# Kernel tuning notes

Measured on AMD Instinct MI355X. Metric: run time of the kernel, lower is better.

The kernel has to match this reference:

```python
import jax, jax.numpy as jnp
import numpy as np
import math

D_MODEL, N_HEADS, D_K, D_V = 512, 2, 64, 64
C_CLIP = 10.0
MASK_FILL = -10.0

def setup_inputs() -> dict:
    key = jax.random.key(0)
    ks = jax.random.split(key, 12)
    B, Lq, Lk = 4, 2048, 2048
    s = 1.0 / math.sqrt(D_MODEL)
    return {
        "Q": jax.random.normal(ks[0], (B, Lq, D_MODEL), jnp.float32),
        "K": jax.random.normal(ks[1], (B, Lk, D_MODEL), jnp.float32),
        "V": jax.random.normal(ks[2], (B, Lk, D_MODEL), jnp.float32),
        "mask": jax.random.randint(ks[3], (B, Lk), 0, 2) > 0,
        "Wq": jax.random.normal(ks[4], (D_MODEL, N_HEADS * D_K), jnp.float32) * s,
        "bq": jnp.zeros((N_HEADS * D_K,), jnp.float32),
        "Wk": jax.random.normal(ks[5], (D_MODEL, N_HEADS * D_K), jnp.float32) * s,
        "bk": jnp.zeros((N_HEADS * D_K,), jnp.float32),
        "Wv": jax.random.normal(ks[6], (D_MODEL, N_HEADS * D_V), jnp.float32) * s,
        "bv": jnp.zeros((N_HEADS * D_V,), jnp.float32),
        "Wo": jax.random.normal(ks[7], (N_HEADS * D_V, D_MODEL), jnp.float32) * s,
        "bo": jnp.zeros((D_MODEL,), jnp.float32),
    }

def reference(Q, K, V, mask, Wq, bq, Wk, bk, Wv, bv, Wo, bo):
    B, Lq, _ = Q.shape
    Lk = K.shape[1]
    # project and split heads: [B, h, L, d]
    q = (Q @ Wq + bq).reshape(B, Lq, N_HEADS, D_K).transpose(0, 2, 1, 3)
    k = (K @ Wk + bk).reshape(B, Lk, N_HEADS, D_K).transpose(0, 2, 1, 3)
    v = (V @ Wv + bv).reshape(B, Lk, N_HEADS, D_V).transpose(0, 2, 1, 3)
    scores = jnp.einsum("bhqd,bhkd->bhqk", q, k) / jnp.sqrt(jnp.float32(D_K))
    scores = jnp.tanh(scores) * C_CLIP
    scores = jnp.where(mask[:, None, None, :], MASK_FILL, scores)
    attn = jax.nn.log_softmax(scores, axis=-1)  # NOTE: log-softmax used directly as weights
    out = jnp.einsum("bhqk,bhkd->bhqd", attn, v)
    out = out.transpose(0, 2, 1, 3).reshape(B, Lq, N_HEADS * D_V)
    out = out @ Wo + bo
    return (out, attn)
```

## Files before the change

kernel.cpp:

```cpp
#include <hip/hip_runtime.h>

typedef __attribute__((ext_vector_type(8))) short short8;
typedef __attribute__((ext_vector_type(4))) float f32x4;

#define DEVI static __device__ __forceinline__

constexpr int NB   = 4;
constexpr int NH   = 2;
constexpr int SEQ  = 2048;
constexpr int DM   = 512;
constexpr int DKV  = 64;
constexpr int HDIM = 128;

DEVI unsigned short f2bf(float f) {
    union { float f; unsigned u; } v; v.f = f;
    unsigned r = v.u + 0x7FFFu + ((v.u >> 16) & 1u);
    return (unsigned short)(r >> 16);
}
DEVI float bf2f(unsigned short s) {
    union { unsigned u; float f; } v; v.u = ((unsigned)s) << 16; return v.f;
}
DEVI void async16(const void* g, void* l) {
    __builtin_amdgcn_global_load_lds(
        (const __attribute__((address_space(1))) unsigned int*)g,
        (__attribute__((address_space(3))) unsigned int*)l, 16, 0, 0);
}

__global__ __launch_bounds__(256) void k_prep(
    const float* __restrict__ Wq, const float* __restrict__ Wk,
    const float* __restrict__ Wv, const float* __restrict__ Wo,
    unsigned short* __restrict__ Wqt, unsigned short* __restrict__ Wkt,
    unsigned short* __restrict__ Wvt, unsigned short* __restrict__ Wot) {
    int id = blockIdx.x * 256 + threadIdx.x;
    int which = id >> 16;
    int rem = id & 65535;
    if (which < 3) {
        const float* W = which == 0 ? Wq : (which == 1 ? Wk : Wv);
        unsigned short* Wt = which == 0 ? Wqt : (which == 1 ? Wkt : Wvt);
        int n = rem >> 9, k = rem & 511;
        Wt[rem] = f2bf(W[k * HDIM + n]);
    } else {
        int n = rem >> 7, k = rem & 127;
        Wot[rem] = f2bf(Wo[k * DM + n]);
    }
}

__global__ __launch_bounds__(256) void k_proj(
    const float* __restrict__ Qg, const float* __restrict__ Kg, const float* __restrict__ Vg,
    const unsigned short* __restrict__ Wqt, const unsigned short* __restrict__ Wkt,
    const unsigned short* __restrict__ Wvt,
    const float* __restrict__ bq, const float* __restrict__ bk, const float* __restrict__ bv,
    unsigned short* __restrict__ qs, unsigned short* __restrict__ kb,
    unsigned short* __restrict__ vt) {
    __shared__ unsigned short lA[64 * 64];
    __shared__ unsigned short lB[128 * 64];

    const int y = blockIdx.y;
    const float* X = y == 0 ? Qg : (y == 1 ? Kg : Vg);
    const unsigned short* Wt = y == 0 ? Wqt : (y == 1 ? Wkt : Wvt);
    const float* bias = y == 0 ? bq : (y == 1 ? bk : bv);
    const float scal = y == 0 ? 0.125f : 1.0f;
    const int row0 = blockIdx.x * 64;
    const int tid = threadIdx.x, lane = tid & 63, wv = tid >> 6;
    const int l16 = lane & 15, lq4 = lane >> 4;
    const int wr = wv >> 1, wc = wv & 1;

    f32x4 acc[2][4];
    #pragma unroll
    for (int i = 0; i < 2; ++i)
        #pragma unroll
        for (int j = 0; j < 4; ++j) acc[i][j] = f32x4{0.f, 0.f, 0.f, 0.f};

    const int arow = tid >> 2, ac0 = (tid & 3) * 16;

    for (int kc = 0; kc < 8; ++kc) {
        {
            const float* src = X + (size_t)(row0 + arow) * DM + kc * 64 + ac0;
            unsigned short* dst = &lA[arow * 64 + ac0];
            #pragma unroll
            for (int i = 0; i < 4; ++i) {
                float4 v = *(const float4*)(src + 4 * i);
                unsigned p0 = (unsigned)f2bf(v.x) | ((unsigned)f2bf(v.y) << 16);
                unsigned p1 = (unsigned)f2bf(v.z) | ((unsigned)f2bf(v.w) << 16);
                *(unsigned*)(dst + 4 * i) = p0;
                *(unsigned*)(dst + 4 * i + 2) = p1;
            }
        }
        #pragma unroll
        for (int c = 0; c < 4; ++c) {
            int chunk = wv * 4 + c;
            int n = chunk * 8 + (lane >> 3);
            int kpart = (lane & 7) * 8;
            const void* g = (const char*)Wt + ((size_t)n * DM + kc * 64 + kpart) * 2;
            void* l = (char*)lB + chunk * 1024 + lane * 16;
            async16(g, l);
        }
        __syncthreads();

        #pragma unroll
        for (int ks = 0; ks < 2; ++ks) {
            short8 a[2], b[4];
            #pragma unroll
            for (int mt = 0; mt < 2; ++mt) {
                int m = wr * 32 + mt * 16 + l16;
                a[mt] = *(const short8*)&lA[m * 64 + ks * 32 + lq4 * 8];
            }
            #pragma unroll
            for (int nt = 0; nt < 4; ++nt) {
                int n = wc * 64 + nt * 16 + l16;
                b[nt] = *(const short8*)&lB[n * 64 + ks * 32 + lq4 * 8];
            }
            #pragma unroll
            for (int mt = 0; mt < 2; ++mt)
                #pragma unroll
                for (int nt = 0; nt < 4; ++nt)
                    acc[mt][nt] = __builtin_amdgcn_mfma_f32_16x16x32_bf16(
                        a[mt], b[nt], acc[mt][nt], 0, 0, 0);
        }
        __syncthreads();
    }

    if (y < 2) {
        unsigned short* dstp = (y == 0) ? qs : kb;
        #pragma unroll
        for (int mt = 0; mt < 2; ++mt)
            #pragma unroll
            for (int nt = 0; nt < 4; ++nt) {
                int col = wc * 64 + nt * 16 + l16;
                float bb = bias[col];
                int h = col >> 6, d = col & 63;
                #pragma unroll
                for (int r = 0; r < 4; ++r) {
                    int row = row0 + wr * 32 + mt * 16 + lq4 * 4 + r;
                    int b = row >> 11, pos = row & 2047;
                    float val = (acc[mt][nt][r] + bb) * scal;
                    dstp[((size_t)(b * NH + h) * SEQ + pos) * DKV + d] = f2bf(val);
                }
            }
    } else {
        #pragma unroll
        for (int mt = 0; mt < 2; ++mt)
            #pragma unroll
            for (int nt = 0; nt < 4; ++nt) {
                int col = wc * 64 + nt * 16 + l16;
                float bb = bias[col];
                #pragma unroll
                for (int r = 0; r < 4; ++r) {
                    int mrow = wr * 32 + mt * 16 + lq4 * 4 + r;
                    lB[col * 64 + mrow] = f2bf(acc[mt][nt][r] + bb);
                }
            }
        __syncthreads();
        int c = tid >> 1, mp = (tid & 1) * 32;
        int b = row0 >> 11, kpos0 = row0 & 2047;
        int h = c >> 6, d = c & 63;
        unsigned short* dst = vt + ((size_t)(b * NH + h) * DKV + d) * SEQ + kpos0 + mp;
        const unsigned short* srcl = &lB[c * 64 + mp];
        #pragma unroll
        for (int i = 0; i < 4; ++i)
            *(uint4*)(dst + 8 * i) = *(const uint4*)(srcl + 8 * i);
    }
}

__global__ __launch_bounds__(256) void k_pass1(
    const unsigned short* __restrict__ qs, const unsigned short* __restrict__ kb,
    const int* __restrict__ maskg, float* __restrict__ Lg) {
    __shared__ unsigned short lK[128 * 64];
    __shared__ int lM[128];
    __shared__ float lsum[32];

    const int bx = blockIdx.x;
    const int qt = bx & 63, bh = bx >> 6;
    const int qbase = qt * 32;
    const int b = bh >> 1;
    const int tid = threadIdx.x, lane = tid & 63, wv = tid >> 6;
    const int l16 = lane & 15, lq4 = lane >> 4;

    if (tid < 32) lsum[tid] = 0.f;

    short8 aq[2][2];
    #pragma unroll
    for (int mt = 0; mt < 2; ++mt)
        #pragma unroll
        for (int ks = 0; ks < 2; ++ks) {
            size_t off = ((size_t)bh * SEQ + qbase + mt * 16 + l16) * DKV + ks * 32 + lq4 * 8;
            aq[mt][ks] = *(const short8*)(qs + off);
        }

    float sums[2][4];
    #pragma unroll
    for (int mt = 0; mt < 2; ++mt)
        #pragma unroll
        for (int r = 0; r < 4; ++r) sums[mt][r] = 0.f;

    const char* kbase_ptr = (const char*)(kb + (size_t)bh * SEQ * DKV);

    for (int kt = 0; kt < 16; ++kt) {
        int kbase = kt * 128;
        #pragma unroll
        for (int c = 0; c < 4; ++c) {
            int chunk = wv * 4 + c;
            const void* g = kbase_ptr + (size_t)kbase * 128 + chunk * 1024 + lane * 16;
            void* l = (char*)lK + chunk * 1024 + lane * 16;
            async16(g, l);
        }
        if (tid < 128) lM[tid] = maskg[b * SEQ + kbase + tid];
        __syncthreads();

        f32x4 acc[2][2];
        #pragma unroll
        for (int mt = 0; mt < 2; ++mt)
            #pragma unroll
            for (int nt = 0; nt < 2; ++nt) acc[mt][nt] = f32x4{0.f, 0.f, 0.f, 0.f};
        #pragma unroll
        for (int ks = 0; ks < 2; ++ks) {
            short8 bfr[2];
            #pragma unroll
            for (int nt = 0; nt < 2; ++nt) {
                int n = wv * 32 + nt * 16 + l16;
                bfr[nt] = *(const short8*)&lK[n * 64 + ks * 32 + lq4 * 8];
            }
            #pragma unroll
            for (int mt = 0; mt < 2; ++mt)
                #pragma unroll
                for (int nt = 0; nt < 2; ++nt)
                    acc[mt][nt] = __builtin_amdgcn_mfma_f32_16x16x32_bf16(
                        aq[mt][ks], bfr[nt], acc[mt][nt], 0, 0, 0);
        }
        #pragma unroll
        for (int nt = 0; nt < 2; ++nt) {
            int col = wv * 32 + nt * 16 + l16;
            int mv = lM[col];
            #pragma unroll
            for (int mt = 0; mt < 2; ++mt)
                #pragma unroll
                for (int r = 0; r < 4; ++r) {
                    float x = acc[mt][nt][r];
                    float e2 = __expf(2.f * x);
                    float s10 = 10.f - 20.f * __builtin_amdgcn_rcpf(1.f + e2);
                    float s = mv ? -10.f : s10;
                    sums[mt][r] += __expf(s);
                }
        }
        __syncthreads();
    }

    #pragma unroll
    for (int mt = 0; mt < 2; ++mt)
        #pragma unroll
        for (int r = 0; r < 4; ++r) {
            float v = sums[mt][r];
            v += __shfl_xor(v, 1); v += __shfl_xor(v, 2);
            v += __shfl_xor(v, 4); v += __shfl_xor(v, 8);
            if (l16 == 0) atomicAdd(&lsum[mt * 16 + lq4 * 4 + r], v);
        }
    __syncthreads();
    if (tid < 32) Lg[(size_t)bh * SEQ + qbase + tid] = __logf(lsum[tid]);
}

__global__ __launch_bounds__(256) void k_pass2(
    const unsigned short* __restrict__ qs, const unsigned short* __restrict__ kb,
    const unsigned short* __restrict__ vt, const int* __restrict__ maskg,
    const float* __restrict__ Lg, float* __restrict__ attnG, float* __restrict__ outh2) {
    __shared__ unsigned short lK[128 * 64];
    __shared__ unsigned short lV[64 * 128];
    __shared__ unsigned short lAttn[64 * 136];
    __shared__ int lM[128];

    const int bx = blockIdx.x;
    const int kh = bx & 1;
    const int rest = bx >> 1;
    const int qt = rest & 31, bh = rest >> 5;
    const int qbase = qt * 64;
    const int b = bh >> 1, h = bh & 1;
    const int tid = threadIdx.x, lane = tid & 63, wv = tid >> 6;
    const int l16 = lane & 15, lq4 = lane >> 4;

    short8 aq[4][2];
    #pragma unroll
    for (int mt = 0; mt < 4; ++mt)
        #pragma unroll
        for (int ks = 0; ks < 2; ++ks) {
            size_t off = ((size_t)bh * SEQ + qbase + mt * 16 + l16) * DKV + ks * 32 + lq4 * 8;
            aq[mt][ks] = *(const short8*)(qs + off);
        }

    float Lr[4][4];
    #pragma unroll
    for (int mt = 0; mt < 4; ++mt)
        #pragma unroll
        for (int r = 0; r < 4; ++r)
            Lr[mt][r] = Lg[(size_t)bh * SEQ + qbase + mt * 16 + lq4 * 4 + r];

    f32x4 o[4];
    #pragma unroll
    for (int mt = 0; mt < 4; ++mt) o[mt] = f32x4{0.f, 0.f, 0.f, 0.f};

    const char* kbase_ptr = (const char*)(kb + (size_t)bh * SEQ * DKV);

    for (int kt = kh * 8; kt < kh * 8 + 8; ++kt) {
        int kbase = kt * 128;
        #pragma unroll
        for (int c = 0; c < 4; ++c) {
            int chunk = wv * 4 + c;
            const void* g = kbase_ptr + (size_t)kbase * 128 + chunk * 1024 + lane * 16;
            void* l = (char*)lK + chunk * 1024 + lane * 16;
            async16(g, l);
        }
        #pragma unroll
        for (int c = 0; c < 4; ++c) {
            int chunk = wv * 4 + c;
            int d = chunk * 4 + (lane >> 4);
            int kk = (lane & 15) * 8;
            const void* g = (const char*)vt + (((size_t)bh * DKV + d) * SEQ + kbase + kk) * 2;
            void* l = (char*)lV + chunk * 1024 + lane * 16;
            async16(g, l);
        }
        if (tid < 128) lM[tid] = maskg[b * SEQ + kbase + tid];
        __syncthreads();

        f32x4 s[4][2];
        #pragma unroll
        for (int mt = 0; mt < 4; ++mt)
            #pragma unroll
            for (int nt = 0; nt < 2; ++nt) s[mt][nt] = f32x4{0.f, 0.f, 0.f, 0.f};
        #pragma unroll
        for (int ks = 0; ks < 2; ++ks) {
            short8 bfr[2];
            #pragma unroll
            for (int nt = 0; nt < 2; ++nt) {
                int n = wv * 32 + nt * 16 + l16;
                bfr[nt] = *(const short8*)&lK[n * 64 + ks * 32 + lq4 * 8];
            }
            #pragma unroll
            for (int mt = 0; mt < 4; ++mt)
                #pragma unroll
                for (int nt = 0; nt < 2; ++nt)
                    s[mt][nt] = __builtin_amdgcn_mfma_f32_16x16x32_bf16(
                        aq[mt][ks], bfr[nt], s[mt][nt], 0, 0, 0);
        }
        #pragma unroll
        for (int nt = 0; nt < 2; ++nt) {
            int col = wv * 32 + nt * 16 + l16;
            int mv = lM[col];
            #pragma unroll
            for (int mt = 0; mt < 4; ++mt)
                #pragma unroll
                for (int r = 0; r < 4; ++r) {
                    float x = s[mt][nt][r];
                    float e2 = __expf(2.f * x);
                    float s10 = 10.f - 20.f * __builtin_amdgcn_rcpf(1.f + e2);
                    float a = (mv ? -10.f : s10) - Lr[mt][r];
                    lAttn[(mt * 16 + lq4 * 4 + r) * 136 + col] = f2bf(a);
                }
        }
        __syncthreads();

        #pragma unroll
        for (int ks = 0; ks < 4; ++ks) {
            short8 bfr = *(const short8*)&lV[(wv * 16 + l16) * 128 + ks * 32 + lq4 * 8];
            #pragma unroll
            for (int mt = 0; mt < 4; ++mt) {
                short8 af = *(const short8*)&lAttn[(mt * 16 + l16) * 136 + ks * 32 + lq4 * 8];
                o[mt] = __builtin_amdgcn_mfma_f32_16x16x32_bf16(af, bfr, o[mt], 0, 0, 0);
            }
        }
        {
            int mrow = tid >> 2, c0 = (tid & 3) * 32;
            float* gdst = attnG + ((size_t)bh * SEQ + qbase + mrow) * SEQ + kbase + c0;
            const unsigned short* srcl = &lAttn[mrow * 136 + c0];
            #pragma unroll
            for (int i = 0; i < 4; ++i) {
                short8 hv = *(const short8*)(srcl + 8 * i);
                float4 f0, f1;
                f0.x = bf2f((unsigned short)hv[0]); f0.y = bf2f((unsigned short)hv[1]);
                f0.z = bf2f((unsigned short)hv[2]); f0.w = bf2f((unsigned short)hv[3]);
                f1.x = bf2f((unsigned short)hv[4]); f1.y = bf2f((unsigned short)hv[5]);
                f1.z = bf2f((unsigned short)hv[6]); f1.w = bf2f((unsigned short)hv[7]);
                *(float4*)(gdst + 8 * i) = f0;
                *(float4*)(gdst + 8 * i + 4) = f1;
            }
        }
        __syncthreads();
    }

    float* dst = outh2 + (size_t)kh * (8192 * 128);
    #pragma unroll
    for (int mt = 0; mt < 4; ++mt)
        #pragma unroll
        for (int r = 0; r < 4; ++r) {
            int q = qbase + mt * 16 + lq4 * 4 + r;
            int dcol = wv * 16 + l16;
            dst[((size_t)b * SEQ + q) * HDIM + h * DKV + dcol] = o[mt][r];
        }
}

__global__ __launch_bounds__(256) void k_comb(const float* __restrict__ outh2,
                                              unsigned short* __restrict__ outh) {
    int i = (blockIdx.x * 256 + threadIdx.x) * 4;
    float4 a = *(const float4*)(outh2 + i);
    float4 c = *(const float4*)(outh2 + 1048576 + i);
    unsigned long long pk =
        (unsigned long long)f2bf(a.x + c.x) |
        ((unsigned long long)f2bf(a.y + c.y) << 16) |
        ((unsigned long long)f2bf(a.z + c.z) << 32) |
        ((unsigned long long)f2bf(a.w + c.w) << 48);
    *(unsigned long long*)(outh + i) = pk;
}

__global__ __launch_bounds__(256) void k_oproj(
    const unsigned short* __restrict__ outh, const unsigned short* __restrict__ Wot,
    const float* __restrict__ bo, float* __restrict__ outG) {
    __shared__ unsigned short lA2[128 * 128];
    __shared__ unsigned short lB2[128 * 128];
    const int row0 = blockIdx.x * 128, col0 = blockIdx.y * 128;
    const int tid = threadIdx.x, lane = tid & 63, wv = tid >> 6;
    const int l16 = lane & 15, lq4 = lane >> 4;
    const int wr = wv >> 1, wc = wv & 1;

    #pragma unroll
    for (int c = 0; c < 8; ++c) {
        int chunk = wv * 8 + c;
        const void* g = (const char*)outh + (size_t)row0 * 256 + chunk * 1024 + lane * 16;
        void* l = (char*)lA2 + chunk * 1024 + lane * 16;
        async16(g, l);
    }
    #pragma unroll
    for (int c = 0; c < 8; ++c) {
        int chunk = wv * 8 + c;
        const void* g = (const char*)Wot + (size_t)col0 * 256 + chunk * 1024 + lane * 16;
        void* l = (char*)lB2 + chunk * 1024 + lane * 16;
        async16(g, l);
    }
    __syncthreads();

    f32x4 acc[4][4];
    #pragma unroll
    for (int mt = 0; mt < 4; ++mt)
        #pragma unroll
        for (int nt = 0; nt < 4; ++nt) acc[mt][nt] = f32x4{0.f, 0.f, 0.f, 0.f};

    #pragma unroll
    for (int ks = 0; ks < 4; ++ks) {
        short8 a[4], bfr[4];
        #pragma unroll
        for (int mt = 0; mt < 4; ++mt)
            a[mt] = *(const short8*)&lA2[(wr * 64 + mt * 16 + l16) * 128 + ks * 32 + lq4 * 8];
        #pragma unroll
        for (int nt = 0; nt < 4; ++nt)
            bfr[nt] = *(const short8*)&lB2[(wc * 64 + nt * 16 + l16) * 128 + ks * 32 + lq4 * 8];
        #pragma unroll
        for (int mt = 0; mt < 4; ++mt)
            #pragma unroll
            for (int nt = 0; nt < 4; ++nt)
                acc[mt][nt] = __builtin_amdgcn_mfma_f32_16x16x32_bf16(
                    a[mt], bfr[nt], acc[mt][nt], 0, 0, 0);
    }

    #pragma unroll
    for (int nt = 0; nt < 4; ++nt) {
        int col = col0 + wc * 64 + nt * 16 + l16;
        float bb = bo[col];
        #pragma unroll
        for (int mt = 0; mt < 4; ++mt)
            #pragma unroll
            for (int r = 0; r < 4; ++r) {
                int row = row0 + wr * 64 + mt * 16 + lq4 * 4 + r;
                outG[(size_t)row * DM + col] = acc[mt][nt][r] + bb;
            }
    }
}

extern "C" void kernel_launch(void* const* d_in, const int* in_sizes, int n_in,
                              void* d_out, int out_size, void* d_ws, size_t ws_size,
                              hipStream_t stream) {
    (void)in_sizes; (void)n_in; (void)out_size; (void)ws_size;
    const float* Qg = (const float*)d_in[0];
    const float* Kg = (const float*)d_in[1];
    const float* Vg = (const float*)d_in[2];
    const int*   maskg = (const int*)d_in[3];
    const float* Wq = (const float*)d_in[4];
    const float* bq = (const float*)d_in[5];
    const float* Wk = (const float*)d_in[6];
    const float* bk = (const float*)d_in[7];
    const float* Wv = (const float*)d_in[8];
    const float* bv = (const float*)d_in[9];
    const float* Wo = (const float*)d_in[10];
    const float* bo = (const float*)d_in[11];

    char* ws = (char*)d_ws;
    unsigned short* qs   = (unsigned short*)(ws);
    unsigned short* kb   = (unsigned short*)(ws + (4  << 20));
    unsigned short* vt   = (unsigned short*)(ws + (8  << 20));
    float*          outh2= (float*)(ws + (12 << 20));
    unsigned short* outh = (unsigned short*)(ws + (20 << 20));
    float*          Lg   = (float*)(ws + (22 << 20));
    unsigned short* Wqt  = (unsigned short*)(ws + (22 << 20) + 65536);
    unsigned short* Wkt  = (unsigned short*)((char*)Wqt + 131072);
    unsigned short* Wvt  = (unsigned short*)((char*)Wkt + 131072);
    unsigned short* Wot  = (unsigned short*)((char*)Wvt + 131072);

    float* outG  = (float*)d_out;
    float* attnG = outG + (size_t)NB * SEQ * DM;

    hipLaunchKernelGGL(k_prep, dim3(1024), dim3(256), 0, stream,
                       Wq, Wk, Wv, Wo, Wqt, Wkt, Wvt, Wot);
    hipLaunchKernelGGL(k_proj, dim3(128, 3), dim3(256), 0, stream,
                       Qg, Kg, Vg, Wqt, Wkt, Wvt, bq, bk, bv, qs, kb, vt);
    hipLaunchKernelGGL(k_pass1, dim3(512), dim3(256), 0, stream, qs, kb, maskg, Lg);
    hipLaunchKernelGGL(k_pass2, dim3(512), dim3(256), 0, stream,
                       qs, kb, vt, maskg, Lg, attnG, outh2);
    hipLaunchKernelGGL(k_comb, dim3(1024), dim3(256), 0, stream, outh2, outh);
    hipLaunchKernelGGL(k_oproj, dim3(64, 4), dim3(256), 0, stream, outh, Wot, bo, outG);
}
```

Baseline: 309.1 us.

## Split key dimension four ways in both attention passes, defer log to pass2

Pass1 now uses 64-row query tiles with a four-way key split. Each block writes partial row sums, which pass2 adds up and takes the log of. Pass2 also splits keys four ways instead of two, and the combine kernel sums four partial outputs. The attention-matrix store is reshaped so each warp writes contiguous 512-byte row segments. The aim is more blocks for better occupancy and more coalesced stores of the large attn output, at the cost of extra partial-output traffic and workspace.

```diff
diff --git a/kernel.cpp b/kernel.cpp
--- a/kernel.cpp
+++ b/kernel.cpp
@@ -1,6 +1,7 @@
 #include <hip/hip_runtime.h>
 
 typedef __attribute__((ext_vector_type(8))) short short8;
+typedef __attribute__((ext_vector_type(4))) short short4v;
 typedef __attribute__((ext_vector_type(4))) float f32x4;
 
 #define DEVI static __device__ __forceinline__
@@ -164,38 +165,38 @@
 
 __global__ __launch_bounds__(256) void k_pass1(
     const unsigned short* __restrict__ qs, const unsigned short* __restrict__ kb,
-    const int* __restrict__ maskg, float* __restrict__ Lg) {
+    const int* __restrict__ maskg, float* __restrict__ Lpart) {
     __shared__ unsigned short lK[128 * 64];
     __shared__ int lM[128];
-    __shared__ float lsum[32];
+    __shared__ float lsumW[4 * 64];
 
     const int bx = blockIdx.x;
-    const int qt = bx & 63, bh = bx >> 6;
-    const int qbase = qt * 32;
+    const int ksp = bx & 3;
+    const int qt = (bx >> 2) & 31;
+    const int bh = bx >> 7;
+    const int qbase = qt * 64;
     const int b = bh >> 1;
     const int tid = threadIdx.x, lane = tid & 63, wv = tid >> 6;
     const int l16 = lane & 15, lq4 = lane >> 4;
 
-    if (tid < 32) lsum[tid] = 0.f;
-
-    short8 aq[2][2];
-    #pragma unroll
-    for (int mt = 0; mt < 2; ++mt)
+    short8 aq[4][2];
+    #pragma unroll
+    for (int mt = 0; mt < 4; ++mt)
         #pragma unroll
         for (int ks = 0; ks < 2; ++ks) {
             size_t off = ((size_t)bh * SEQ + qbase + mt * 16 + l16) * DKV + ks * 32 + lq4 * 8;
             aq[mt][ks] = *(const short8*)(qs + off);
         }
 
-    float sums[2][4];
-    #pragma unroll
-    for (int mt = 0; mt < 2; ++mt)
+    float sums[4][4];
+    #pragma unroll
+    for (int mt = 0; mt < 4; ++mt)
         #pragma unroll
         for (int r = 0; r < 4; ++r) sums[mt][r] = 0.f;
 
     const char* kbase_ptr = (const char*)(kb + (size_t)bh * SEQ * DKV);
 
-    for (int kt = 0; kt < 16; ++kt) {
+    for (int kt = ksp * 4; kt < ksp * 4 + 4; ++kt) {
         int kbase = kt * 128;
         #pragma unroll
         for (int c = 0; c < 4; ++c) {
@@ -207,9 +208,9 @@
         if (tid < 128) lM[tid] = maskg[b * SEQ + kbase + tid];
         __syncthreads();
 
-        f32x4 acc[2][2];
-        #pragma unroll
-        for (int mt = 0; mt < 2; ++mt)
+        f32x4 acc[4][2];
+        #pragma unroll
+        for (int mt = 0; mt < 4; ++mt)
             #pragma unroll
             for (int nt = 0; nt < 2; ++nt) acc[mt][nt] = f32x4{0.f, 0.f, 0.f, 0.f};
         #pragma unroll
@@ -221,7 +222,7 @@
                 bfr[nt] = *(const short8*)&lK[n * 64 + ks * 32 + lq4 * 8];
             }
             #pragma unroll
-            for (int mt = 0; mt < 2; ++mt)
+            for (int mt = 0; mt < 4; ++mt)
                 #pragma unroll
                 for (int nt = 0; nt < 2; ++nt)
                     acc[mt][nt] = __builtin_amdgcn_mfma_f32_16x16x32_bf16(
@@ -232,7 +233,7 @@
             int col = wv * 32 + nt * 16 + l16;
             int mv = lM[col];
             #pragma unroll
-            for (int mt = 0; mt < 2; ++mt)
+            for (int mt = 0; mt < 4; ++mt)
                 #pragma unroll
                 for (int r = 0; r < 4; ++r) {
                     float x = acc[mt][nt][r];
@@ -246,31 +247,34 @@
     }
 
     #pragma unroll
-    for (int mt = 0; mt < 2; ++mt)
+    for (int mt = 0; mt < 4; ++mt)
         #pragma unroll
         for (int r = 0; r < 4; ++r) {
             float v = sums[mt][r];
             v += __shfl_xor(v, 1); v += __shfl_xor(v, 2);
             v += __shfl_xor(v, 4); v += __shfl_xor(v, 8);
-            if (l16 == 0) atomicAdd(&lsum[mt * 16 + lq4 * 4 + r], v);
+            if (l16 == 0) lsumW[wv * 64 + mt * 16 + lq4 * 4 + r] = v;
         }
     __syncthreads();
-    if (tid < 32) Lg[(size_t)bh * SEQ + qbase + tid] = __logf(lsum[tid]);
+    if (tid < 64) {
+        float v = lsumW[tid] + lsumW[64 + tid] + lsumW[128 + tid] + lsumW[192 + tid];
+        Lpart[(size_t)ksp * (8 * SEQ) + (size_t)bh * SEQ + qbase + tid] = v;
+    }
 }
 
 __global__ __launch_bounds__(256) void k_pass2(
     const unsigned short* __restrict__ qs, const unsigned short* __restrict__ kb,
     const unsigned short* __restrict__ vt, const int* __restrict__ maskg,
-    const float* __restrict__ Lg, float* __restrict__ attnG, float* __restrict__ outh2) {
+    const float* __restrict__ Lpart, float* __restrict__ attnG, float* __restrict__ outh2) {
     __shared__ unsigned short lK[128 * 64];
     __shared__ unsigned short lV[64 * 128];
     __shared__ unsigned short lAttn[64 * 136];
     __shared__ int lM[128];
 
     const int bx = blockIdx.x;
-    const int kh = bx & 1;
-    const int rest = bx >> 1;
-    const int qt = rest & 31, bh = rest >> 5;
+    const int ksp = bx & 3;
+    const int qt = (bx >> 2) & 31;
+    const int bh = bx >> 7;
     const int qbase = qt * 64;
     const int b = bh >> 1, h = bh & 1;
     const int tid = threadIdx.x, lane = tid & 63, wv = tid >> 6;
@@ -289,8 +293,12 @@
     #pragma unroll
     for (int mt = 0; mt < 4; ++mt)
         #pragma unroll
-        for (int r = 0; r < 4; ++r)
-            Lr[mt][r] = Lg[(size_t)bh * SEQ + qbase + mt * 16 + lq4 * 4 + r];
+        for (int r = 0; r < 4; ++r) {
+            size_t idx = (size_t)bh * SEQ + qbase + mt * 16 + lq4 * 4 + r;
+            float s = Lpart[idx] + Lpart[8 * SEQ + idx] +
+                      Lpart[2 * 8 * SEQ + idx] + Lpart[3 * 8 * SEQ + idx];
+            Lr[mt][r] = __logf(s);
+        }
 
     f32x4 o[4];
     #pragma unroll
@@ -298,7 +306,7 @@
 
     const char* kbase_ptr = (const char*)(kb + (size_t)bh * SEQ * DKV);
 
-    for (int kt = kh * 8; kt < kh * 8 + 8; ++kt) {
+    for (int kt = ksp * 4; kt < ksp * 4 + 4; ++kt) {
         int kbase = kt * 128;
         #pragma unroll
         for (int c = 0; c < 4; ++c) {
@@ -365,26 +373,21 @@
                 o[mt] = __builtin_amdgcn_mfma_f32_16x16x32_bf16(af, bfr, o[mt], 0, 0, 0);
             }
         }
-        {
-            int mrow = tid >> 2, c0 = (tid & 3) * 32;
-            float* gdst = attnG + ((size_t)bh * SEQ + qbase + mrow) * SEQ + kbase + c0;
-            const unsigned short* srcl = &lAttn[mrow * 136 + c0];
-            #pragma unroll
-            for (int i = 0; i < 4; ++i) {
-                short8 hv = *(const short8*)(srcl + 8 * i);
-                float4 f0, f1;
-                f0.x = bf2f((unsigned short)hv[0]); f0.y = bf2f((unsigned short)hv[1]);
-                f0.z = bf2f((unsigned short)hv[2]); f0.w = bf2f((unsigned short)hv[3]);
-                f1.x = bf2f((unsigned short)hv[4]); f1.y = bf2f((unsigned short)hv[5]);
-                f1.z = bf2f((unsigned short)hv[6]); f1.w = bf2f((unsigned short)hv[7]);
-                *(float4*)(gdst + 8 * i) = f0;
-                *(float4*)(gdst + 8 * i + 4) = f1;
-            }
-        }
-        __syncthreads();
-    }
-
-    float* dst = outh2 + (size_t)kh * (8192 * 128);
+        #pragma unroll
+        for (int j = 0; j < 8; ++j) {
+            int row = j * 8 + (tid >> 5);
+            int col = (tid & 31) * 4;
+            short4v hv = *(const short4v*)&lAttn[row * 136 + col];
+            float4 f;
+            f.x = bf2f((unsigned short)hv[0]); f.y = bf2f((unsigned short)hv[1]);
+            f.z = bf2f((unsigned short)hv[2]); f.w = bf2f((unsigned short)hv[3]);
+            float* gdst = attnG + ((size_t)bh * SEQ + qbase + row) * SEQ + kbase + col;
+            *(float4*)gdst = f;
+        }
+        __syncthreads();
+    }
+
+    float* dst = outh2 + (size_t)ksp * (8192 * HDIM);
     #pragma unroll
     for (int mt = 0; mt < 4; ++mt)
         #pragma unroll
@@ -400,11 +403,13 @@
     int i = (blockIdx.x * 256 + threadIdx.x) * 4;
     float4 a = *(const float4*)(outh2 + i);
     float4 c = *(const float4*)(outh2 + 1048576 + i);
+    float4 d = *(const float4*)(outh2 + 2 * 1048576 + i);
+    float4 e = *(const float4*)(outh2 + 3 * 1048576 + i);
     unsigned long long pk =
-        (unsigned long long)f2bf(a.x + c.x) |
-        ((unsigned long long)f2bf(a.y + c.y) << 16) |
-        ((unsigned long long)f2bf(a.z + c.z) << 32) |
-        ((unsigned long long)f2bf(a.w + c.w) << 48);
+        (unsigned long long)f2bf(a.x + c.x + d.x + e.x) |
+        ((unsigned long long)f2bf(a.y + c.y + d.y + e.y) << 16) |
+        ((unsigned long long)f2bf(a.z + c.z + d.z + e.z) << 32) |
+        ((unsigned long long)f2bf(a.w + c.w + d.w + e.w) << 48);
     *(unsigned long long*)(outh + i) = pk;
 }
 
@@ -493,9 +498,9 @@
     unsigned short* kb   = (unsigned short*)(ws + (4  << 20));
     unsigned short* vt   = (unsigned short*)(ws + (8  << 20));
     float*          outh2= (float*)(ws + (12 << 20));
-    unsigned short* outh = (unsigned short*)(ws + (20 << 20));
-    float*          Lg   = (float*)(ws + (22 << 20));
-    unsigned short* Wqt  = (unsigned short*)(ws + (22 << 20) + 65536);
+    unsigned short* outh = (unsigned short*)(ws + (28 << 20));
+    float*          Lpart= (float*)(ws + (30 << 20));
+    unsigned short* Wqt  = (unsigned short*)(ws + (30 << 20) + 262144);
     unsigned short* Wkt  = (unsigned short*)((char*)Wqt + 131072);
     unsigned short* Wvt  = (unsigned short*)((char*)Wkt + 131072);
     unsigned short* Wot  = (unsigned short*)((char*)Wvt + 131072);
@@ -507,9 +512,9 @@
                        Wq, Wk, Wv, Wo, Wqt, Wkt, Wvt, Wot);
     hipLaunchKernelGGL(k_proj, dim3(128, 3), dim3(256), 0, stream,
                        Qg, Kg, Vg, Wqt, Wkt, Wvt, bq, bk, bv, qs, kb, vt);
-    hipLaunchKernelGGL(k_pass1, dim3(512), dim3(256), 0, stream, qs, kb, maskg, Lg);
-    hipLaunchKernelGGL(k_pass2, dim3(512), dim3(256), 0, stream,
-                       qs, kb, vt, maskg, Lg, attnG, outh2);
+    hipLaunchKernelGGL(k_pass1, dim3(1024), dim3(256), 0, stream, qs, kb, maskg, Lpart);
+    hipLaunchKernelGGL(k_pass2, dim3(1024), dim3(256), 0, stream,
+                       qs, kb, vt, maskg, Lpart, attnG, outh2);
     hipLaunchKernelGGL(k_comb, dim3(1024), dim3(256), 0, stream, outh2, outh);
     hipLaunchKernelGGL(k_oproj, dim3(64, 4), dim3(256), 0, stream, outh, Wot, bo, outG);
 }
```

Result: faster. 261.7 us (-15.3%).
